# Optimization experiments

Measured on AMD Instinct MI355X. Metric: run time of the kernel, lower is better.

Reference implementation:

```python
import jax, jax.numpy as jnp
import numpy as np

B, D, H, S, C = 8192, 1024, 2048, 4, 1000
PARTIAL_NORM = 1.5
SELF_MOD_STEPS = 2
TOPK = 64
EPS = 1e-08


def setup_inputs() -> dict:
    key = jax.random.key(0)
    ks = jax.random.split(key, 8)
    x = jax.random.normal(ks[0], (B, D), dtype=jnp.float32)
    # wavefunction nets: torch Linear(D, 2H) -> weight [2H, D]; stacked over S
    lim_w = 1.0 / np.sqrt(D)
    Wnet = jax.random.uniform(ks[1], (S, 2 * H, D), jnp.float32, -lim_w, lim_w)
    bnet = jax.random.uniform(ks[2], (S, 2 * H), jnp.float32, -lim_w, lim_w)
    phases = jnp.zeros((S, 1), dtype=jnp.float32)
    lim_g = 1.0 / np.sqrt(H)
    Wg = jax.random.uniform(ks[3], (H, H), jnp.float32, -lim_g, lim_g)
    bg = jax.random.uniform(ks[4], (H,), jnp.float32, -lim_g, lim_g)
    Wc = jax.random.uniform(ks[5], (C, H), jnp.float32, -lim_g, lim_g)
    bc = jnp.zeros((C,), dtype=jnp.float32).at[1].set(0.75)
    return {"x": x, "Wnet": Wnet, "bnet": bnet, "phases": phases,
            "Wg": Wg, "bg": bg, "Wc": Wc, "bc": bc}


def reference(x, Wnet, bnet, phases, Wg, bg, Wc, bc):
    # all wavefunction linears at once: [B, S, 2H]
    z = jnp.einsum('bd,sod->bso', x, Wnet) + bnet[None, :, :]
    out = jnp.exp(-(z * z))
    alpha, beta = out[..., :H], out[..., H:]  # [B, S, H]
    norm_sq = jnp.sum(alpha * alpha + beta * beta, axis=-1, keepdims=True) + EPS
    factor = jnp.sqrt(PARTIAL_NORM ** 2 / norm_sq)
    alpha = alpha * factor
    beta = beta * factor
    ph = phases[None, :, :]  # [1, S, 1] broadcast (phase_per_dim=False)
    c, s_ = jnp.cos(ph), jnp.sin(ph)
    real_stack = alpha * c - beta * s_  # [B, S, H]
    imag_stack = alpha * s_ + beta * c
    # interference softmax via cosine similarity to mean wave
    mean_real = jnp.mean(real_stack, axis=1)  # [B, H]
    mean_norm = jnp.sqrt(jnp.sum(mean_real ** 2, axis=1, keepdims=True)) + EPS  # [B,1]
    wave_norms = jnp.sqrt(jnp.sum(real_stack ** 2, axis=2)) + EPS  # [B, S]
    dot = jnp.einsum('bsh,bh->bs', real_stack, mean_real)
    cosine_sim = dot / (wave_norms * mean_norm)
    w = jax.nn.softmax(cosine_sim, axis=1)[..., None]  # [B, S, 1]
    sup_real = jnp.sum(real_stack * w, axis=1)  # [B, H]
    sup_imag = jnp.sum(imag_stack * w, axis=1)
    # sequential sigmoid gating
    for _ in range(SELF_MOD_STEPS):
        mag = jnp.sqrt(sup_real ** 2 + sup_imag ** 2 + EPS)
        gate = jax.nn.sigmoid(mag @ Wg.T + bg)
        sup_real = sup_real * gate
        sup_imag = sup_imag * gate
    mag_sq = sup_real ** 2 + sup_imag ** 2
    # topk mask + normalize
    _, inds = jax.lax.top_k(mag_sq, TOPK)  # [B, k]
    rows = jnp.arange(mag_sq.shape[0])[:, None]
    mask = jnp.zeros_like(mag_sq).at[rows, inds].set(1.0)
    masked = mag_sq * mask
    probs = masked / (jnp.sum(masked, axis=1, keepdims=True) + EPS)
    return probs @ Wc.T + bc
```

## Files before the change

kernel.cpp:

```cpp
#include <hip/hip_runtime.h>
#include <hip/hip_bf16.h>
#include <cstdint>
#include <cstddef>

#define B_SZ 8192
#define D_SZ 1024
#define H_SZ 2048
#define S_SZ 4
#define C_SZ 1000
#define N1   16384
#define EPSF 1e-8f

typedef __attribute__((ext_vector_type(4))) float f32x4;
typedef __attribute__((ext_vector_type(8))) short s16x8;

typedef __attribute__((address_space(3))) void lds_void;
typedef const __attribute__((address_space(1))) void glb_void;

static __device__ __forceinline__ void gload16(const void* g, void* l){
  __builtin_amdgcn_global_load_lds((glb_void*)g, (lds_void*)l, 16, 0, 0);
}

static __device__ __forceinline__ float bf2f(unsigned short u){
  union { unsigned int i; float f; } c; c.i = ((unsigned int)u) << 16; return c.f;
}
static __device__ __forceinline__ unsigned short f2bf(float f){
  union { float f; unsigned int i; } c; c.f = f;
  unsigned int x = c.i;
  return (unsigned short)((x + 0x7FFFu + ((x >> 16) & 1u)) >> 16);
}

__global__ __launch_bounds__(256) void cvt_bf16(const float* __restrict__ src,
                                                unsigned short* __restrict__ dst, int n4){
  int i = blockIdx.x * 256 + threadIdx.x;
  if (i >= n4) return;
  float4 v = ((const float4*)src)[i];
  ushort4 o; o.x = f2bf(v.x); o.y = f2bf(v.y); o.z = f2bf(v.z); o.w = f2bf(v.w);
  ((ushort4*)dst)[i] = o;
}

__global__ __launch_bounds__(256) void transpose_wc(const float* __restrict__ Wc,
                                                    unsigned short* __restrict__ WcTb){
  int idx = blockIdx.x * 256 + threadIdx.x;
  if (idx >= H_SZ * C_SZ) return;
  int h = idx / C_SZ, c = idx - h * C_SZ;
  WcTb[idx] = f2bf(Wc[(size_t)c * H_SZ + h]);
}

#define BM 128
#define BN 128
#define BK 64

template<int MODE>
__global__ __launch_bounds__(256) void gemm_bt(
    const unsigned short* __restrict__ A,
    const unsigned short* __restrict__ Bm,
    int M, int N, int K,
    const float* __restrict__ bias,
    unsigned short* __restrict__ Gout,
    unsigned short* __restrict__ supR,
    unsigned short* __restrict__ supI,
    unsigned short* __restrict__ magout)
{
  __shared__ __align__(16) unsigned short lds[2*BM*BK];
  unsigned short* la = lds;
  unsigned short* lb = lds + BM*BK;
  const int tid = threadIdx.x;
  const int lane = tid & 63;
  const int w = tid >> 6;
  const int wm = w >> 1, wn = w & 1;
  const int lr = lane & 15, lg = lane >> 4;
  const int srow = lane >> 3;
  const int scol = (lane & 7) * 8;

  const int gx = gridDim.x;
  const int nwg = gx * gridDim.y;
  const int bid = blockIdx.y * gx + blockIdx.x;
  const int q = nwg >> 3, rmd = nwg & 7, xcd = bid & 7, lid = bid >> 3;
  const int swz = (xcd < rmd ? xcd*(q+1) : rmd*(q+1) + (xcd-rmd)*q) + lid;
  const int m0 = (swz / gx) * BM;
  const int n0 = (swz % gx) * BN;

  f32x4 acc[4][4];
  #pragma unroll
  for (int i = 0; i < 4; i++)
    #pragma unroll
    for (int j = 0; j < 4; j++){ f32x4 z = {0.f,0.f,0.f,0.f}; acc[i][j] = z; }

  const int nkt = K / BK;
  for (int kt = 0; kt < nkt; ++kt){
    __syncthreads();
    const unsigned short* ga = A  + (size_t)m0*K + (size_t)kt*BK;
    const unsigned short* gb = Bm + (size_t)n0*K + (size_t)kt*BK;
    #pragma unroll
    for (int i = 0; i < 4; i++){
      int seg = i*4 + w;
      gload16(ga + (size_t)(seg*8 + srow)*K + scol, &la[seg*512]);
      gload16(gb + (size_t)(seg*8 + srow)*K + scol, &lb[seg*512]);
    }
    __syncthreads();
    #pragma unroll
    for (int kk = 0; kk < 2; ++kk){
      s16x8 af[4], bfr[4];
      #pragma unroll
      for (int mi = 0; mi < 4; mi++)
        af[mi] = *(const s16x8*)&la[(wm*64 + mi*16 + lr)*BK + kk*32 + lg*8];
      #pragma unroll
      for (int ni = 0; ni < 4; ni++)
        bfr[ni] = *(const s16x8*)&lb[(wn*64 + ni*16 + lr)*BK + kk*32 + lg*8];
      #pragma unroll
      for (int mi = 0; mi < 4; mi++)
        #pragma unroll
        for (int ni = 0; ni < 4; ni++)
          acc[mi][ni] = __builtin_amdgcn_mfma_f32_16x16x32_bf16(af[mi], bfr[ni], acc[mi][ni], 0, 0, 0);
    }
  }

  __syncthreads();
  unsigned short* ct = lds;
  #pragma unroll
  for (int mi = 0; mi < 4; mi++){
    #pragma unroll
    for (int ni = 0; ni < 4; ni++){
      int ncol = wn*64 + ni*16 + lr;
      float bn = bias[n0 + ncol];
      #pragma unroll
      for (int r = 0; r < 4; r++){
        int mrow = wm*64 + mi*16 + lg*4 + r;
        float v = acc[mi][ni][r] + bn;
        unsigned short o;
        if (MODE == 0) o = f2bf(expf(-v*v));
        else           o = f2bf(1.0f / (1.0f + expf(-v)));
        ct[mrow*128 + ncol] = o;
      }
    }
  }
  __syncthreads();
  #pragma unroll
  for (int i = 0; i < 8; i++){
    int e = (i*256 + tid) * 8;
    int row = e >> 7, col = e & 127;
    if (MODE == 0){
      *(uint4*)&Gout[(size_t)(m0+row)*N + n0+col] = *(const uint4*)&ct[e];
    } else {
      size_t gi = (size_t)(m0+row)*N + n0+col;
      s16x8 gt = *(const s16x8*)&ct[e];
      s16x8 rr = *(const s16x8*)&supR[gi];
      s16x8 qq = *(const s16x8*)&supI[gi];
      s16x8 ro, io, mo;
      #pragma unroll
      for (int j = 0; j < 8; j++){
        float g  = bf2f((unsigned short)gt[j]);
        float rf = bf2f((unsigned short)rr[j]) * g;
        float qf = bf2f((unsigned short)qq[j]) * g;
        ro[j] = (short)f2bf(rf);
        io[j] = (short)f2bf(qf);
        mo[j] = (short)f2bf(sqrtf(rf*rf + qf*qf + EPSF));
      }
      *(s16x8*)&supR[gi] = ro;
      *(s16x8*)&supI[gi] = io;
      *(s16x8*)&magout[gi] = mo;
    }
  }
}

template<int NR>
__device__ __forceinline__ void breduce(const float* vals, float* red,
                                        float* outp, int lane, int wid, int tid){
  #pragma unroll
  for (int j = 0; j < NR; j++){
    float x = vals[j];
    #pragma unroll
    for (int off = 32; off >= 1; off >>= 1) x += __shfl_down(x, off, 64);
    if (lane == 0) red[wid*NR + j] = x;
  }
  __syncthreads();
  if (tid < NR) outp[tid] = red[tid] + red[NR+tid] + red[2*NR+tid] + red[3*NR+tid];
  __syncthreads();
}

__global__ __launch_bounds__(256) void k2_superpose(
  const unsigned short* __restrict__ G, const float* __restrict__ phases,
  unsigned short* __restrict__ supR, unsigned short* __restrict__ supI,
  unsigned short* __restrict__ mag)
{
  __shared__ float red[36];
  __shared__ float outp[9];
  const int tid = threadIdx.x, lane = tid & 63, wid = tid >> 6;
  const int b = blockIdx.x;
  const size_t gbase = (size_t)b * N1;
  const int h0 = tid * 8;

  float av[S_SZ][8], bv[S_SZ][8], nsq[S_SZ];
  #pragma unroll
  for (int s = 0; s < S_SZ; s++){
    s16x8 va = *(const s16x8*)&G[gbase + s*4096 + h0];
    s16x8 vb = *(const s16x8*)&G[gbase + s*4096 + 2048 + h0];
    float accn = 0.f;
    #pragma unroll
    for (int i = 0; i < 8; i++){
      float a  = bf2f((unsigned short)va[i]);
      float bb = bf2f((unsigned short)vb[i]);
      av[s][i] = a; bv[s][i] = bb;
      accn += a*a + bb*bb;
    }
    nsq[s] = accn;
  }
  breduce<4>(nsq, red, outp, lane, wid, tid);

  float fac[S_SZ], cc[S_SZ], sn[S_SZ];
  #pragma unroll
  for (int s = 0; s < S_SZ; s++){
    fac[s] = sqrtf(2.25f / (outp[s] + EPSF));
    float ph = phases[s];
    cc[s] = cosf(ph); sn[s] = sinf(ph);
  }
  float re[S_SZ][8], im[S_SZ][8], mr[8];
  #pragma unroll
  for (int i = 0; i < 8; i++) mr[i] = 0.f;
  #pragma unroll
  for (int s = 0; s < S_SZ; s++)
    #pragma unroll
    for (int i = 0; i < 8; i++){
      float r = fac[s]*(av[s][i]*cc[s] - bv[s][i]*sn[s]);
      float qv = fac[s]*(av[s][i]*sn[s] + bv[s][i]*cc[s]);
      re[s][i] = r; im[s][i] = qv; mr[i] += r;
    }
  #pragma unroll
  for (int i = 0; i < 8; i++) mr[i] *= 0.25f;

  float pv[9];
  { float t = 0.f;
    #pragma unroll
    for (int i = 0; i < 8; i++) t += mr[i]*mr[i];
    pv[0] = t; }
  #pragma unroll
  for (int s = 0; s < S_SZ; s++){
    float t1 = 0.f, t2 = 0.f;
    #pragma unroll
    for (int i = 0; i < 8; i++){ t1 += re[s][i]*re[s][i]; t2 += re[s][i]*mr[i]; }
    pv[1+s] = t1; pv[5+s] = t2;
  }
  breduce<9>(pv, red, outp, lane, wid, tid);

  float mean_norm = sqrtf(outp[0]) + EPSF;
  float wv[S_SZ]; float mx = -1e30f;
  #pragma unroll
  for (int s = 0; s < S_SZ; s++){
    float wn = sqrtf(outp[1+s]) + EPSF;
    float csim = outp[5+s] / (wn * mean_norm);
    wv[s] = csim; mx = fmaxf(mx, csim);
  }
  float se = 0.f;
  #pragma unroll
  for (int s = 0; s < S_SZ; s++){ wv[s] = expf(wv[s]-mx); se += wv[s]; }
  float invse = 1.f / se;
  #pragma unroll
  for (int s = 0; s < S_SZ; s++) wv[s] *= invse;

  s16x8 ro, io, mo;
  #pragma unroll
  for (int i = 0; i < 8; i++){
    float sr = 0.f, si = 0.f;
    #pragma unroll
    for (int s = 0; s < S_SZ; s++){ sr += wv[s]*re[s][i]; si += wv[s]*im[s][i]; }
    ro[i] = (short)f2bf(sr); io[i] = (short)f2bf(si);
    mo[i] = (short)f2bf(sqrtf(sr*sr + si*si + EPSF));
  }
  size_t ob = (size_t)b*H_SZ + h0;
  *(s16x8*)&supR[ob] = ro;
  *(s16x8*)&supI[ob] = io;
  *(s16x8*)&mag[ob]  = mo;
}

__global__ __launch_bounds__(256) void k4_topk(
  const unsigned short* __restrict__ supR, const unsigned short* __restrict__ supI,
  const unsigned short* __restrict__ WcTb, const float* __restrict__ bcv,
  float* __restrict__ outg)
{
  __shared__ float msq[H_SZ];
  __shared__ int   redi[4];
  __shared__ int   sel_idx[64];
  __shared__ float sel_p[64];
  __shared__ int   cnt;
  __shared__ float ssum_sh;
  const int tid = threadIdx.x, lane = tid & 63, wid = tid >> 6;
  const int b = blockIdx.x;
  const size_t base = (size_t)b * H_SZ;

  if (tid < 64){ sel_p[tid] = 0.f; sel_idx[tid] = 0; }
  if (tid == 0) cnt = 0;

  float v[8]; unsigned int u[8];
  {
    s16x8 r = *(const s16x8*)&supR[base + tid*8];
    s16x8 qv = *(const s16x8*)&supI[base + tid*8];
    #pragma unroll
    for (int i = 0; i < 8; i++){
      float rf = bf2f((unsigned short)r[i]);
      float qf = bf2f((unsigned short)qv[i]);
      v[i] = rf*rf + qf*qf;
    }
  }
  #pragma unroll
  for (int i = 0; i < 8; i++){ msq[tid*8+i] = v[i]; u[i] = __float_as_uint(v[i]); }
  __syncthreads();

  unsigned int lo = 0u, hi = 0xFFFFFFFFu;
  for (int it = 0; it < 32; ++it){
    unsigned int mid = (unsigned int)(((unsigned long long)lo + (unsigned long long)hi + 1ull) >> 1);
    int c = 0;
    #pragma unroll
    for (int i = 0; i < 8; i++) c += (u[i] >= mid) ? 1 : 0;
    #pragma unroll
    for (int off = 32; off >= 1; off >>= 1) c += __shfl_down(c, off, 64);
    if (lane == 0) redi[wid] = c;
    __syncthreads();
    int total = redi[0]+redi[1]+redi[2]+redi[3];
    __syncthreads();
    if (total >= 64) lo = mid; else hi = mid - 1u;
  }
  const unsigned int V = lo;

  int cg = 0;
  #pragma unroll
  for (int i = 0; i < 8; i++) cg += (u[i] > V) ? 1 : 0;
  #pragma unroll
  for (int off = 32; off >= 1; off >>= 1) cg += __shfl_down(cg, off, 64);
  if (lane == 0) redi[wid] = cg;
  __syncthreads();
  const int ng = redi[0]+redi[1]+redi[2]+redi[3];
  const int kfill = 64 - ng;

  #pragma unroll
  for (int i = 0; i < 8; i++){
    if (u[i] > V){
      int ppos = atomicAdd(&cnt, 1);
      if (ppos < 64){ sel_idx[ppos] = tid*8 + i; sel_p[ppos] = v[i]; }
    }
  }
  __syncthreads();
  if (wid == 0){
    int taken = 0;
    for (int b2 = 0; b2 < H_SZ; b2 += 64){
      float val = msq[b2 + lane];
      bool eq = (__float_as_uint(val) == V);
      unsigned long long mk = __ballot(eq);
      int pre = __popcll(mk & ((1ull << lane) - 1ull));
      int dst = ng + taken + pre;
      if (eq && dst < 64){
        sel_idx[dst] = b2 + lane;
        sel_p [dst] = val;
      }
      taken += __popcll(mk);
      if (taken >= kfill) break;
    }
  }
  __syncthreads();
  if (wid == 0){
    float xx = sel_p[lane];
    #pragma unroll
    for (int off = 32; off >= 1; off >>= 1) xx += __shfl_down(xx, off, 64);
    if (lane == 0) ssum_sh = xx;
  }
  __syncthreads();
  const float invden = 1.f / (ssum_sh + EPSF);
  if (tid < 64) sel_p[tid] *= invden;
  __syncthreads();

  for (int c = tid; c < C_SZ; c += 256){
    float acc = bcv[c];
    #pragma unroll 8
    for (int k = 0; k < 64; k++) acc += sel_p[k] * bf2f(WcTb[(size_t)sel_idx[k]*C_SZ + c]);
    outg[(size_t)b*C_SZ + c] = acc;
  }
}

extern "C" void kernel_launch(void* const* d_in, const int* in_sizes, int n_in,
                              void* d_out, int out_size, void* d_ws, size_t ws_size,
                              hipStream_t stream){
  (void)in_sizes; (void)n_in; (void)out_size;
  const float* x      = (const float*)d_in[0];
  const float* Wnet   = (const float*)d_in[1];
  const float* bnet   = (const float*)d_in[2];
  const float* phases = (const float*)d_in[3];
  const float* Wg     = (const float*)d_in[4];
  const float* bg     = (const float*)d_in[5];
  const float* Wc     = (const float*)d_in[6];
  const float* bc     = (const float*)d_in[7];
  float* out = (float*)d_out;

  char* p = (char*)d_ws;
  const size_t MB = 1024ull*1024ull;
  unsigned short* xb    = (unsigned short*)(p + 0);
  unsigned short* Wnetb = (unsigned short*)(p + 16*MB);
  unsigned short* Wgb   = (unsigned short*)(p + 0);
  unsigned short* WcTb  = (unsigned short*)(p + 8*MB);
  unsigned short* supR  = (unsigned short*)(p + 48*MB);
  unsigned short* supI  = (unsigned short*)(p + 80*MB);
  unsigned short* mag   = (unsigned short*)(p + 112*MB);
  unsigned short* G     = (unsigned short*)(p + 144*MB);

  size_t avail = (ws_size > 144*MB) ? (ws_size - 144*MB) : 0;
  long rows_cap = (long)(avail / ((size_t)N1 * 2));
  int chunk = (int)((rows_cap / BM) * BM);
  if (chunk > B_SZ) chunk = B_SZ;
  if (chunk < BM)   chunk = BM;

  cvt_bf16<<<(B_SZ*D_SZ/4 + 255)/256, 256, 0, stream>>>(x, xb, B_SZ*D_SZ/4);
  cvt_bf16<<<(N1*D_SZ/4 + 255)/256, 256, 0, stream>>>(Wnet, Wnetb, N1*D_SZ/4);

  for (int b0 = 0; b0 < B_SZ; b0 += chunk){
    int rows = (B_SZ - b0 < chunk) ? (B_SZ - b0) : chunk;
    gemm_bt<0><<<dim3(N1/BN, rows/BM), 256, 0, stream>>>(
        xb + (size_t)b0*D_SZ, Wnetb, rows, N1, D_SZ, bnet, G, nullptr, nullptr, nullptr);
    k2_superpose<<<rows, 256, 0, stream>>>(
        G, phases, supR + (size_t)b0*H_SZ, supI + (size_t)b0*H_SZ, mag + (size_t)b0*H_SZ);
  }

  cvt_bf16<<<(H_SZ*H_SZ/4 + 255)/256, 256, 0, stream>>>(Wg, Wgb, H_SZ*H_SZ/4);
  transpose_wc<<<(H_SZ*C_SZ + 255)/256, 256, 0, stream>>>(Wc, WcTb);

  gemm_bt<1><<<dim3(H_SZ/BN, B_SZ/BM), 256, 0, stream>>>(
      mag, Wgb, B_SZ, H_SZ, H_SZ, bg, nullptr, supR, supI, mag);
  gemm_bt<1><<<dim3(H_SZ/BN, B_SZ/BM), 256, 0, stream>>>(
      mag, Wgb, B_SZ, H_SZ, H_SZ, bg, nullptr, supR, supI, mag);

  k4_topk<<<B_SZ, 256, 0, stream>>>(supR, supI, WcTb, bc, out);
}
```

Before: 1.177 ms.

## Double-buffer GEMM LDS tiles and XOR-swizzle columns to avoid bank conflicts

The bf16 MFMA GEMM now uses two LDS buffers, so the global-to-LDS loads for the next K tile are issued before computing on the current tile, with one waitcnt and barrier per iteration instead of two syncs. It also applies an XOR swizzle to the 16-byte chunk index within each row, both when storing via global_load_lds and when reading fragments, which is meant to cut LDS bank conflicts. The cost is doubled LDS use (64KB), which may lower occupancy.

```diff
diff --git a/kernel.cpp b/kernel.cpp
--- a/kernel.cpp
+++ b/kernel.cpp
@@ -50,6 +50,7 @@
 #define BM 128
 #define BN 128
 #define BK 64
+#define TILE_ES (BM*BK)
 
 template<int MODE>
 __global__ __launch_bounds__(256) void gemm_bt(
@@ -62,16 +63,14 @@
     unsigned short* __restrict__ supI,
     unsigned short* __restrict__ magout)
 {
-  __shared__ __align__(16) unsigned short lds[2*BM*BK];
-  unsigned short* la = lds;
-  unsigned short* lb = lds + BM*BK;
+  __shared__ __align__(16) unsigned short lds[2*2*TILE_ES];
   const int tid = threadIdx.x;
   const int lane = tid & 63;
   const int w = tid >> 6;
   const int wm = w >> 1, wn = w & 1;
   const int lr = lane & 15, lg = lane >> 4;
   const int srow = lane >> 3;
-  const int scol = (lane & 7) * 8;
+  const int scol = ((lane & 7) ^ (lane >> 3)) * 8;
 
   const int gx = gridDim.x;
   const int nwg = gx * gridDim.y;
@@ -81,6 +80,9 @@
   const int m0 = (swz / gx) * BM;
   const int n0 = (swz % gx) * BN;
 
+  const unsigned short* gaBase = A  + (size_t)m0*K + (size_t)(srow)*K + scol;
+  const unsigned short* gbBase = Bm + (size_t)n0*K + (size_t)(srow)*K + scol;
+
   f32x4 acc[4][4];
   #pragma unroll
   for (int i = 0; i < 4; i++)
@@ -88,35 +90,55 @@
     for (int j = 0; j < 4; j++){ f32x4 z = {0.f,0.f,0.f,0.f}; acc[i][j] = z; }
 
   const int nkt = K / BK;
+
+  #define STAGE(bi, kt) do {                                                   \
+    unsigned short* la_ = lds + (bi)*2*TILE_ES;                                \
+    unsigned short* lb_ = la_ + TILE_ES;                                       \
+    const size_t ko_ = (size_t)(kt)*BK;                                        \
+    _Pragma("unroll")                                                          \
+    for (int i_ = 0; i_ < 4; i_++){                                            \
+      int seg_ = i_*4 + w;                                                     \
+      gload16(gaBase + (size_t)(seg_*8)*K + ko_, &la_[seg_*512]);              \
+      gload16(gbBase + (size_t)(seg_*8)*K + ko_, &lb_[seg_*512]);              \
+    }                                                                          \
+  } while(0)
+
+  STAGE(0, 0);
+  asm volatile("s_waitcnt vmcnt(0)" ::: "memory");
+  __builtin_amdgcn_s_barrier();
+
+  int cur = 0;
   for (int kt = 0; kt < nkt; ++kt){
-    __syncthreads();
-    const unsigned short* ga = A  + (size_t)m0*K + (size_t)kt*BK;
-    const unsigned short* gb = Bm + (size_t)n0*K + (size_t)kt*BK;
-    #pragma unroll
-    for (int i = 0; i < 4; i++){
-      int seg = i*4 + w;
-      gload16(ga + (size_t)(seg*8 + srow)*K + scol, &la[seg*512]);
-      gload16(gb + (size_t)(seg*8 + srow)*K + scol, &lb[seg*512]);
-    }
-    __syncthreads();
+    if (kt + 1 < nkt) STAGE(cur ^ 1, kt + 1);
+    const unsigned short* la = lds + cur*2*TILE_ES;
+    const unsigned short* lb = la + TILE_ES;
     #pragma unroll
     for (int kk = 0; kk < 2; ++kk){
       s16x8 af[4], bfr[4];
       #pragma unroll
-      for (int mi = 0; mi < 4; mi++)
-        af[mi] = *(const s16x8*)&la[(wm*64 + mi*16 + lr)*BK + kk*32 + lg*8];
+      for (int mi = 0; mi < 4; mi++){
+        int row = wm*64 + mi*16 + lr;
+        int ch  = (kk*4 + lg) ^ (lr & 7);
+        af[mi] = *(const s16x8*)&la[row*BK + ch*8];
+      }
       #pragma unroll
-      for (int ni = 0; ni < 4; ni++)
-        bfr[ni] = *(const s16x8*)&lb[(wn*64 + ni*16 + lr)*BK + kk*32 + lg*8];
+      for (int ni = 0; ni < 4; ni++){
+        int row = wn*64 + ni*16 + lr;
+        int ch  = (kk*4 + lg) ^ (lr & 7);
+        bfr[ni] = *(const s16x8*)&lb[row*BK + ch*8];
+      }
       #pragma unroll
       for (int mi = 0; mi < 4; mi++)
         #pragma unroll
         for (int ni = 0; ni < 4; ni++)
           acc[mi][ni] = __builtin_amdgcn_mfma_f32_16x16x32_bf16(af[mi], bfr[ni], acc[mi][ni], 0, 0, 0);
     }
-  }
-
-  __syncthreads();
+    asm volatile("s_waitcnt vmcnt(0)" ::: "memory");
+    __builtin_amdgcn_s_barrier();
+    cur ^= 1;
+  }
+  #undef STAGE
+
   unsigned short* ct = lds;
   #pragma unroll
   for (int mi = 0; mi < 4; mi++){
```

Result: faster. 1.033 ms (-12.3%).

## Replace GEMM with 256x256-tile, 8-wave, double-buffered swizzled-LDS pipelined kernel

Applied to the files above, without the earlier changes.

Replaces the 128x128 single-stage GEMM with a 256x256 tile kernel using 8 waves, double-buffered LDS with XOR-swizzled layout, and interleaved prefetch of the next K tiles between MFMA phases, with setprio hints. The goal is to raise arithmetic intensity per tile, hide global load latency behind MFMA work, and avoid LDS bank conflicts. It uses 128KB LDS per block and more accumulator registers, and the larger tiles give fewer blocks for the chunked first GEMM.

```diff
diff --git a/kernel.cpp b/kernel.cpp
--- a/kernel.cpp
+++ b/kernel.cpp
@@ -47,12 +47,9 @@
   WcTb[idx] = f2bf(Wc[(size_t)c * H_SZ + h]);
 }
 
-#define BM 128
-#define BN 128
-#define BK 64
 
 template<int MODE>
-__global__ __launch_bounds__(256) void gemm_bt(
+__global__ __launch_bounds__(512, 2) void gemm8(
     const unsigned short* __restrict__ A,
     const unsigned short* __restrict__ Bm,
     int M, int N, int K,
@@ -62,89 +59,161 @@
     unsigned short* __restrict__ supI,
     unsigned short* __restrict__ magout)
 {
-  __shared__ __align__(16) unsigned short lds[2*BM*BK];
-  unsigned short* la = lds;
-  unsigned short* lb = lds + BM*BK;
+  __shared__ __align__(16) unsigned short lds[65536];
   const int tid = threadIdx.x;
   const int lane = tid & 63;
   const int w = tid >> 6;
-  const int wm = w >> 1, wn = w & 1;
+  const int wm = w >> 2, wn = w & 3;
   const int lr = lane & 15, lg = lane >> 4;
-  const int srow = lane >> 3;
-  const int scol = (lane & 7) * 8;
+  const int rowq = lane >> 3;
+  const int sc8 = ((lane & 7) ^ rowq) * 8;
+  const int ch0 = (0*4 + lg) ^ (lr & 7);
+  const int ch1 = (1*4 + lg) ^ (lr & 7);
 
   const int gx = gridDim.x;
   const int nwg = gx * gridDim.y;
   const int bid = blockIdx.y * gx + blockIdx.x;
   const int q = nwg >> 3, rmd = nwg & 7, xcd = bid & 7, lid = bid >> 3;
   const int swz = (xcd < rmd ? xcd*(q+1) : rmd*(q+1) + (xcd-rmd)*q) + lid;
-  const int m0 = (swz / gx) * BM;
-  const int n0 = (swz % gx) * BN;
-
-  f32x4 acc[4][4];
-  #pragma unroll
-  for (int i = 0; i < 4; i++)
+  const int m0 = (swz / gx) * 256;
+  const int n0 = (swz % gx) * 256;
+
+  const unsigned short* ga = A  + (size_t)m0*K;
+  const unsigned short* gb = Bm + (size_t)n0*K;
+
+  f32x4 acc[8][4];
+  #pragma unroll
+  for (int i = 0; i < 8; i++)
     #pragma unroll
     for (int j = 0; j < 4; j++){ f32x4 z = {0.f,0.f,0.f,0.f}; acc[i][j] = z; }
 
-  const int nkt = K / BK;
-  for (int kt = 0; kt < nkt; ++kt){
-    __syncthreads();
-    const unsigned short* ga = A  + (size_t)m0*K + (size_t)kt*BK;
-    const unsigned short* gb = Bm + (size_t)n0*K + (size_t)kt*BK;
-    #pragma unroll
-    for (int i = 0; i < 4; i++){
-      int seg = i*4 + w;
-      gload16(ga + (size_t)(seg*8 + srow)*K + scol, &la[seg*512]);
-      gload16(gb + (size_t)(seg*8 + srow)*K + scol, &lb[seg*512]);
-    }
-    __syncthreads();
-    #pragma unroll
-    for (int kk = 0; kk < 2; ++kk){
-      s16x8 af[4], bfr[4];
-      #pragma unroll
-      for (int mi = 0; mi < 4; mi++)
-        af[mi] = *(const s16x8*)&la[(wm*64 + mi*16 + lr)*BK + kk*32 + lg*8];
-      #pragma unroll
-      for (int ni = 0; ni < 4; ni++)
-        bfr[ni] = *(const s16x8*)&lb[(wn*64 + ni*16 + lr)*BK + kk*32 + lg*8];
-      #pragma unroll
-      for (int mi = 0; mi < 4; mi++)
-        #pragma unroll
-        for (int ni = 0; ni < 4; ni++)
-          acc[mi][ni] = __builtin_amdgcn_mfma_f32_16x16x32_bf16(af[mi], bfr[ni], acc[mi][ni], 0, 0, 0);
-    }
-  }
-
-  __syncthreads();
-  unsigned short* ct = lds;
-  #pragma unroll
-  for (int mi = 0; mi < 4; mi++){
-    #pragma unroll
-    for (int ni = 0; ni < 4; ni++){
-      int ncol = wn*64 + ni*16 + lr;
+  auto stage_half = [&](const unsigned short* base, int half, int kt, int ldsbase){
+    #pragma unroll
+    for (int j = 0; j < 2; j++){
+      int seg = j*8 + w;
+      const unsigned short* g = base + (size_t)(half*128 + seg*8 + rowq)*K + kt*64 + sc8;
+      gload16(g, &lds[ldsbase + half*8192 + seg*512]);
+    }
+  };
+
+  const int nkt = K >> 6;
+
+  stage_half(ga, 0, 0, 0);      stage_half(ga, 1, 0, 0);
+  stage_half(gb, 0, 0, 16384);  stage_half(gb, 1, 0, 16384);
+  stage_half(ga, 0, 1, 32768);  stage_half(ga, 1, 1, 32768);
+  asm volatile("s_waitcnt vmcnt(0)" ::: "memory");
+  __builtin_amdgcn_s_barrier();
+
+  for (int t = 0; t < nkt; ++t){
+    const int bo = (t & 1) << 15;
+    const int bn = 32768 - bo;
+    s16x8 a03[4][2], a47[4][2], bfr[4][2];
+
+    #pragma unroll
+    for (int f = 0; f < 4; f++){
+      int r = wm*128 + f*16 + lr;
+      a03[f][0] = *(const s16x8*)&lds[bo + r*64 + ch0*8];
+      a03[f][1] = *(const s16x8*)&lds[bo + r*64 + ch1*8];
+    }
+    #pragma unroll
+    for (int nf = 0; nf < 4; nf++){
+      int r = wn*64 + nf*16 + lr;
+      bfr[nf][0] = *(const s16x8*)&lds[bo + 16384 + r*64 + ch0*8];
+      bfr[nf][1] = *(const s16x8*)&lds[bo + 16384 + r*64 + ch1*8];
+    }
+    if (t + 1 < nkt) stage_half(gb, 0, t+1, bn + 16384);
+    __builtin_amdgcn_s_barrier();
+    asm volatile("s_waitcnt lgkmcnt(0)" ::: "memory");
+    __builtin_amdgcn_sched_barrier(0);
+    __builtin_amdgcn_s_setprio(1);
+    #pragma unroll
+    for (int f = 0; f < 4; f++)
+      #pragma unroll
+      for (int nf = 0; nf < 2; nf++){
+        acc[f][nf] = __builtin_amdgcn_mfma_f32_16x16x32_bf16(a03[f][0], bfr[nf][0], acc[f][nf], 0,0,0);
+        acc[f][nf] = __builtin_amdgcn_mfma_f32_16x16x32_bf16(a03[f][1], bfr[nf][1], acc[f][nf], 0,0,0);
+      }
+    __builtin_amdgcn_s_setprio(0);
+    __builtin_amdgcn_s_barrier();
+
+    #pragma unroll
+    for (int f = 0; f < 4; f++){
+      int r = wm*128 + 64 + f*16 + lr;
+      a47[f][0] = *(const s16x8*)&lds[bo + r*64 + ch0*8];
+      a47[f][1] = *(const s16x8*)&lds[bo + r*64 + ch1*8];
+    }
+    if (t + 1 < nkt) stage_half(gb, 1, t+1, bn + 16384);
+    __builtin_amdgcn_s_barrier();
+    asm volatile("s_waitcnt lgkmcnt(0)" ::: "memory");
+    __builtin_amdgcn_sched_barrier(0);
+    __builtin_amdgcn_s_setprio(1);
+    #pragma unroll
+    for (int f = 0; f < 4; f++)
+      #pragma unroll
+      for (int nf = 2; nf < 4; nf++){
+        acc[f][nf] = __builtin_amdgcn_mfma_f32_16x16x32_bf16(a03[f][0], bfr[nf][0], acc[f][nf], 0,0,0);
+        acc[f][nf] = __builtin_amdgcn_mfma_f32_16x16x32_bf16(a03[f][1], bfr[nf][1], acc[f][nf], 0,0,0);
+      }
+    __builtin_amdgcn_s_setprio(0);
+    __builtin_amdgcn_s_barrier();
+
+    if (t + 2 < nkt) stage_half(ga, 0, t+2, bo);
+    __builtin_amdgcn_s_barrier();
+    __builtin_amdgcn_s_setprio(1);
+    #pragma unroll
+    for (int f = 0; f < 4; f++)
+      #pragma unroll
+      for (int nf = 0; nf < 2; nf++){
+        acc[4+f][nf] = __builtin_amdgcn_mfma_f32_16x16x32_bf16(a47[f][0], bfr[nf][0], acc[4+f][nf], 0,0,0);
+        acc[4+f][nf] = __builtin_amdgcn_mfma_f32_16x16x32_bf16(a47[f][1], bfr[nf][1], acc[4+f][nf], 0,0,0);
+      }
+    __builtin_amdgcn_s_setprio(0);
+    __builtin_amdgcn_s_barrier();
+
+    if (t + 2 < nkt) stage_half(ga, 1, t+2, bo);
+    __builtin_amdgcn_s_barrier();
+    __builtin_amdgcn_s_setprio(1);
+    #pragma unroll
+    for (int f = 0; f < 4; f++)
+      #pragma unroll
+      for (int nf = 2; nf < 4; nf++){
+        acc[4+f][nf] = __builtin_amdgcn_mfma_f32_16x16x32_bf16(a47[f][0], bfr[nf][0], acc[4+f][nf], 0,0,0);
+        acc[4+f][nf] = __builtin_amdgcn_mfma_f32_16x16x32_bf16(a47[f][1], bfr[nf][1], acc[4+f][nf], 0,0,0);
+      }
+    __builtin_amdgcn_s_setprio(0);
+    asm volatile("s_waitcnt vmcnt(4)" ::: "memory");
+    __builtin_amdgcn_s_barrier();
+  }
+
+  asm volatile("s_waitcnt vmcnt(0)" ::: "memory");
+  __builtin_amdgcn_s_barrier();
+  #pragma unroll
+  for (int f = 0; f < 8; f++){
+    #pragma unroll
+    for (int nf = 0; nf < 4; nf++){
+      int ncol = wn*64 + nf*16 + lr;
       float bn = bias[n0 + ncol];
       #pragma unroll
       for (int r = 0; r < 4; r++){
-        int mrow = wm*64 + mi*16 + lg*4 + r;
-        float v = acc[mi][ni][r] + bn;
+        int mrow = wm*128 + f*16 + lg*4 + r;
+        float v = acc[f][nf][r] + bn;
         unsigned short o;
         if (MODE == 0) o = f2bf(expf(-v*v));
         else           o = f2bf(1.0f / (1.0f + expf(-v)));
-        ct[mrow*128 + ncol] = o;
-      }
-    }
-  }
-  __syncthreads();
-  #pragma unroll
-  for (int i = 0; i < 8; i++){
-    int e = (i*256 + tid) * 8;
-    int row = e >> 7, col = e & 127;
+        lds[mrow*256 + ncol] = o;
+      }
+    }
+  }
+  __syncthreads();
+  #pragma unroll
+  for (int i = 0; i < 16; i++){
+    int e = (i*512 + tid) * 8;
+    int row = e >> 8, col = e & 255;
     if (MODE == 0){
-      *(uint4*)&Gout[(size_t)(m0+row)*N + n0+col] = *(const uint4*)&ct[e];
+      *(uint4*)&Gout[(size_t)(m0+row)*N + n0+col] = *(const uint4*)&lds[e];
     } else {
       size_t gi = (size_t)(m0+row)*N + n0+col;
-      s16x8 gt = *(const s16x8*)&ct[e];
+      s16x8 gt = *(const s16x8*)&lds[e];
       s16x8 rr = *(const s16x8*)&supR[gi];
       s16x8 qq = *(const s16x8*)&supI[gi];
       s16x8 ro, io, mo;
@@ -403,16 +472,16 @@
 
   size_t avail = (ws_size > 144*MB) ? (ws_size - 144*MB) : 0;
   long rows_cap = (long)(avail / ((size_t)N1 * 2));
-  int chunk = (int)((rows_cap / BM) * BM);
+  int chunk = (int)((rows_cap / 256) * 256);
   if (chunk > B_SZ) chunk = B_SZ;
-  if (chunk < BM)   chunk = BM;
+  if (chunk < 256)  chunk = 256;
 
   cvt_bf16<<<(B_SZ*D_SZ/4 + 255)/256, 256, 0, stream>>>(x, xb, B_SZ*D_SZ/4);
   cvt_bf16<<<(N1*D_SZ/4 + 255)/256, 256, 0, stream>>>(Wnet, Wnetb, N1*D_SZ/4);
 
   for (int b0 = 0; b0 < B_SZ; b0 += chunk){
     int rows = (B_SZ - b0 < chunk) ? (B_SZ - b0) : chunk;
-    gemm_bt<0><<<dim3(N1/BN, rows/BM), 256, 0, stream>>>(
+    gemm8<0><<<dim3(N1/256, rows/256), 512, 0, stream>>>(
         xb + (size_t)b0*D_SZ, Wnetb, rows, N1, D_SZ, bnet, G, nullptr, nullptr, nullptr);
     k2_superpose<<<rows, 256, 0, stream>>>(
         G, phases, supR + (size_t)b0*H_SZ, supI + (size_t)b0*H_SZ, mag + (size_t)b0*H_SZ);
@@ -421,9 +490,9 @@
   cvt_bf16<<<(H_SZ*H_SZ/4 + 255)/256, 256, 0, stream>>>(Wg, Wgb, H_SZ*H_SZ/4);
   transpose_wc<<<(H_SZ*C_SZ + 255)/256, 256, 0, stream>>>(Wc, WcTb);
 
-  gemm_bt<1><<<dim3(H_SZ/BN, B_SZ/BM), 256, 0, stream>>>(
+  gemm8<1><<<dim3(H_SZ/256, B_SZ/256), 512, 0, stream>>>(
       mag, Wgb, B_SZ, H_SZ, H_SZ, bg, nullptr, supR, supI, mag);
-  gemm_bt<1><<<dim3(H_SZ/BN, B_SZ/BM), 256, 0, stream>>>(
+  gemm8<1><<<dim3(H_SZ/256, B_SZ/256), 512, 0, stream>>>(
       mag, Wgb, B_SZ, H_SZ, H_SZ, bg, nullptr, supR, supI, mag);
 
   k4_topk<<<B_SZ, 256, 0, stream>>>(supR, supI, WcTb, bc, out);
```

Measured after the change: 987.0 us. 16.2% less time.
